# Kernel optimization log

Measured on AMD Instinct MI355X. Metric: run time of the kernel, lower is better.

## Reference

```python
import jax, jax.numpy as jnp
import numpy as np

B, N, C = 4, 2048, 320
H, D = 5, 64            # heads, dim_head
INNER = H * D           # 320


def setup_inputs() -> dict:
    key = jax.random.key(0)
    ks = jax.random.split(key, 7)
    x = jax.random.normal(ks[0], (B, N, C), dtype=jnp.float32)
    edge = jax.random.uniform(ks[1], (B, N, 1), dtype=jnp.float32)
    s = 1.0 / np.sqrt(C)
    Wq = jax.random.normal(ks[2], (C, INNER), dtype=jnp.float32) * s
    Wk = jax.random.normal(ks[3], (C, INNER), dtype=jnp.float32) * s
    Wv = jax.random.normal(ks[4], (C, INNER), dtype=jnp.float32) * s
    Wo = jax.random.normal(ks[5], (INNER, C), dtype=jnp.float32) * (1.0 / np.sqrt(INNER))
    bo = jnp.zeros((C,), dtype=jnp.float32)
    return {"x": x, "edge": edge, "Wq": Wq, "Wk": Wk, "Wv": Wv, "Wo": Wo, "bo": bo}


def _split_heads(t):
    # 'b n (h d) -> (b h) n d'  (batch-major, head-minor)
    b, n, _ = t.shape
    return t.reshape(b, n, H, D).transpose(0, 2, 1, 3).reshape(b * H, n, D)


def reference(x, edge, Wq, Wk, Wv, Wo, bo):
    scale = D ** -0.5
    q = _split_heads(x @ Wq).astype(jnp.float32)   # (B*H, N, D)
    k = _split_heads(x @ Wk).astype(jnp.float32)
    v = _split_heads(x @ Wv)

    sim = jnp.einsum('bid,bjd->bij', q, k) * scale  # (B*H, N, N)

    # torch: edge.repeat(h, 1, 1) -> batch-minor tiling; index i uses edge[i % B]
    edge_rep = jnp.tile(edge, (H, 1, 1))            # (H*B, N, 1)
    edge_matrix = edge_rep * edge_rep.transpose(0, 2, 1)  # outer product (H*B, N, N)

    sim = jax.nn.softmax(sim * edge_matrix, axis=-1)
    out = jnp.einsum('bij,bjd->bid', sim, v)        # (B*H, N, D)

    # '(b h) n d -> b n (h d)'
    out = out.reshape(B, H, N, D).transpose(0, 2, 1, 3).reshape(B, N, INNER)
    return out @ Wo + bo
```

## Files before the change

### kernel.cpp

```cpp
#include <hip/hip_runtime.h>
#include <hip/hip_bf16.h>
#include <math.h>


typedef short bf16x8 __attribute__((ext_vector_type(8)));
typedef float f32x4 __attribute__((ext_vector_type(4)));

static __device__ __forceinline__ ushort f2bf(float f) {
  union { float f; unsigned u; } v; v.f = f;
  unsigned r = (v.u + 0x7fffu + ((v.u >> 16) & 1u)) >> 16;
  return (ushort)r;
}
static __device__ __forceinline__ float fexp2(float x) {
#if __has_builtin(__builtin_amdgcn_exp2f)
  return __builtin_amdgcn_exp2f(x);
#else
  return exp2f(x);
#endif
}
static __device__ __forceinline__ f32x4 mfma32(bf16x8 a, bf16x8 b, f32x4 c) {
  return __builtin_amdgcn_mfma_f32_16x16x32_bf16(a, b, c, 0, 0, 0);
}

__global__ __launch_bounds__(256) void prep_kernel(
    const float* __restrict__ x,
    const float* __restrict__ Wq, const float* __restrict__ Wk,
    const float* __restrict__ Wv, const float* __restrict__ Wo,
    ushort* __restrict__ xb, ushort* __restrict__ wt)
{
  const int w = blockIdx.x;
  if (w < 2560) {
    const int t = threadIdx.x;
    const int mt2 = w / 5;
    const int kc = (w % 5) * 2 + (t >> 7);
    const int f = (t & 127) * 4;
    const int qq = f >> 7, mm = (f >> 3) & 15, e0 = f & 7;
    float4 v = *reinterpret_cast<const float4*>(
        x + (size_t)(mt2 * 16 + mm) * 320 + kc * 32 + qq * 8 + e0);
    ushort4 o = { f2bf(v.x), f2bf(v.y), f2bf(v.z), f2bf(v.w) };
    *reinterpret_cast<ushort4*>(xb + (size_t)(mt2 * 10 + kc) * 512 + f) = o;
  } else {
    const int w2 = w - 2560;
    const int nt2 = w2 % 20, kc = (w2 / 20) % 10, z = w2 / 200;
    const float* W = z == 0 ? Wq : z == 1 ? Wk : z == 2 ? Wv : Wo;
    const int f = threadIdx.x * 2;
    const int qq = f >> 7, nn = (f >> 3) & 15, e0 = f & 7;
    const int k = kc * 32 + qq * 8 + e0, n = nt2 * 16 + nn;
    float v0 = W[(size_t)k * 320 + n];
    float v1 = W[(size_t)(k + 1) * 320 + n];
    ushort2 o = { f2bf(v0), f2bf(v1) };
    *reinterpret_cast<ushort2*>(
        wt + (size_t)z * 102400 + (size_t)(nt2 * 10 + kc) * 512 + f) = o;
  }
}

__global__ __launch_bounds__(256, 3) void qkv_gemm(
    const ushort* __restrict__ xb, const float* __restrict__ edge,
    const ushort* __restrict__ wt,
    ushort* __restrict__ qp, ushort* __restrict__ kS, ushort* __restrict__ vS)
{
  const int w = blockIdx.x;
  const int s = (w & 7) * 60 + (w >> 3);
  const int mg = s / 15, zh = s % 15;
  const int z = zh / 5, h = zh % 5;
  const int wave = threadIdx.x >> 6, lane = threadIdx.x & 63;
  const int m16 = lane & 15, quad = lane >> 4;
  const int m0 = mg * 256 + wave * 64;
  const ushort* atile = xb + (size_t)(m0 >> 4) * 5120 + lane * 8;
  const ushort* btile = wt + (size_t)z * 102400 + (size_t)(h * 4) * 5120 + lane * 8;

  f32x4 acc[4][4];
#pragma unroll
  for (int i = 0; i < 4; ++i)
#pragma unroll
    for (int ns = 0; ns < 4; ++ns) acc[i][ns] = (f32x4){0.f, 0.f, 0.f, 0.f};

#pragma unroll
  for (int kc = 0; kc < 10; ++kc) {
    bf16x8 af[4], bf[4];
#pragma unroll
    for (int i = 0; i < 4; ++i)
      af[i] = *reinterpret_cast<const bf16x8*>(atile + (i * 10 + kc) * 512);
#pragma unroll
    for (int ns = 0; ns < 4; ++ns)
      bf[ns] = *reinterpret_cast<const bf16x8*>(btile + (ns * 10 + kc) * 512);
    if (z == 2) {
#pragma unroll
      for (int i = 0; i < 4; ++i)
#pragma unroll
        for (int ns = 0; ns < 4; ++ns)
          acc[i][ns] = mfma32(af[i], bf[ns], acc[i][ns]);
    } else {
#pragma unroll
      for (int i = 0; i < 4; ++i)
#pragma unroll
        for (int ns = 0; ns < 4; ++ns)
          acc[i][ns] = mfma32(bf[ns], af[i], acc[i][ns]);
    }
  }

  const float QSCALE = 0.18033688011112042f;
  const int b = m0 >> 11;
  const int bh = b * 5 + h;
  const float* eb = edge + (size_t)((b + h) & 3) * 2048;
  const int nwb = m0 & 2047;

  if (z == 0) {
#pragma unroll
    for (int i = 0; i < 4; ++i) {
      const int n = nwb + i * 16 + m16;
      const float e = eb[n] * QSCALE;
      ushort* dst = qp + ((size_t)bh * 2048 + n) * 64 + quad * 4;
#pragma unroll
      for (int ns = 0; ns < 4; ++ns) {
        ushort4 o = { f2bf(acc[i][ns][0] * e), f2bf(acc[i][ns][1] * e),
                      f2bf(acc[i][ns][2] * e), f2bf(acc[i][ns][3] * e) };
        *reinterpret_cast<ushort4*>(dst + ns * 16) = o;
      }
    }
  } else if (z == 1) {
#pragma unroll
    for (int i = 0; i < 4; ++i) {
      const int j = nwb + i * 16 + m16;
      const float e = eb[j];
      const size_t base = (size_t)bh * 131072 +
                          (size_t)((m0 >> 4) + i & 127) * 1024;
#pragma unroll
      for (int ns = 0; ns < 4; ++ns) {
        size_t a0 = base + (ns >> 1) * 512 +
                    ((((ns * 2 + (quad >> 1)) & 3) * 16 + m16)) * 8 +
                    (quad & 1) * 4;
        ushort4 o = { f2bf(acc[i][ns][0] * e), f2bf(acc[i][ns][1] * e),
                      f2bf(acc[i][ns][2] * e), f2bf(acc[i][ns][3] * e) };
        *reinterpret_cast<ushort4*>(kS + a0) = o;
      }
    }
  } else {
    const int jb = nwb >> 6;
#pragma unroll
    for (int i = 0; i < 4; ++i) {
      const int kb = i >> 1, e4 = (i & 1) * 4;
#pragma unroll
      for (int ns = 0; ns < 4; ++ns) {
        ushort4 o = { f2bf(acc[i][ns][0]), f2bf(acc[i][ns][1]),
                      f2bf(acc[i][ns][2]), f2bf(acc[i][ns][3]) };
        size_t addr = (size_t)bh * 131072 + (size_t)ns * 32768 +
                      (size_t)jb * 1024 + kb * 512 +
                      (quad * 16 + m16) * 8 + e4;
        *reinterpret_cast<ushort4*>(vS + addr) = o;
      }
    }
  }
}

__global__ __launch_bounds__(256, 3) void attn_kernel(
    const ushort* __restrict__ qp, const ushort* __restrict__ kS,
    const ushort* __restrict__ vS, ushort* __restrict__ ao)
{
  __shared__ f32x4 lo[3][16][64];
  __shared__ float lrs[4][4][16];
  const int w = blockIdx.x;
  const int s = (w & 7) * 80 + (w >> 3);
  const int bh = s >> 5, qt = s & 31;
  const int b = bh / 5, h = bh % 5;
  const int wave = threadIdx.x >> 6, lane = threadIdx.x & 63;
  const int m16 = lane & 15, quad = lane >> 4;
  const int q0 = qt * 64;

  bf16x8 qf[4][2];
#pragma unroll
  for (int qs = 0; qs < 4; ++qs) {
    const ushort* qrow = qp + ((size_t)bh * 2048 + q0 + qs * 16 + m16) * 64;
    qf[qs][0] = *reinterpret_cast<const bf16x8*>(qrow + quad * 8);
    qf[qs][1] = *reinterpret_cast<const bf16x8*>(qrow + 32 + quad * 8);
  }
  const ushort* kb_p = kS + (size_t)bh * 131072 + (size_t)wave * 32768 + lane * 8;
  const ushort* vb_p = vS + (size_t)bh * 131072 + (size_t)wave * 8192 + lane * 8;

  f32x4 oacc[4][4];
  float rs[4];
#pragma unroll
  for (int qs = 0; qs < 4; ++qs) {
    rs[qs] = 0.f;
#pragma unroll
    for (int dt = 0; dt < 4; ++dt) oacc[qs][dt] = (f32x4){0.f, 0.f, 0.f, 0.f};
  }

#pragma unroll 2
  for (int u = 0; u < 16; ++u) {
    bf16x8 kf[2][2], vf[4];
#pragma unroll
    for (int ss = 0; ss < 2; ++ss)
#pragma unroll
      for (int hf = 0; hf < 2; ++hf)
        kf[ss][hf] = *reinterpret_cast<const bf16x8*>(
            kb_p + (size_t)u * 2048 + ss * 1024 + hf * 512);
#pragma unroll
    for (int dt = 0; dt < 4; ++dt)
      vf[dt] = *reinterpret_cast<const bf16x8*>(
          vb_p + (size_t)dt * 32768 + (size_t)u * 512);

#pragma unroll
    for (int qs = 0; qs < 4; ++qs) {
      f32x4 st0 = (f32x4){0.f, 0.f, 0.f, 0.f};
      f32x4 st1 = (f32x4){0.f, 0.f, 0.f, 0.f};
      st0 = mfma32(kf[0][0], qf[qs][0], st0);
      st0 = mfma32(kf[0][1], qf[qs][1], st0);
      st1 = mfma32(kf[1][0], qf[qs][0], st1);
      st1 = mfma32(kf[1][1], qf[qs][1], st1);
      unsigned b0 = __float_as_uint(fexp2(st0[0]));
      unsigned b1 = __float_as_uint(fexp2(st0[1]));
      unsigned b2 = __float_as_uint(fexp2(st0[2]));
      unsigned b3 = __float_as_uint(fexp2(st0[3]));
      unsigned b4 = __float_as_uint(fexp2(st1[0]));
      unsigned b5 = __float_as_uint(fexp2(st1[1]));
      unsigned b6 = __float_as_uint(fexp2(st1[2]));
      unsigned b7 = __float_as_uint(fexp2(st1[3]));
      float t0 = __uint_as_float(b0 & 0xffff0000u);
      float t1 = __uint_as_float(b1 & 0xffff0000u);
      float t2 = __uint_as_float(b2 & 0xffff0000u);
      float t3 = __uint_as_float(b3 & 0xffff0000u);
      float t4 = __uint_as_float(b4 & 0xffff0000u);
      float t5 = __uint_as_float(b5 & 0xffff0000u);
      float t6 = __uint_as_float(b6 & 0xffff0000u);
      float t7 = __uint_as_float(b7 & 0xffff0000u);
      rs[qs] += ((t0 + t1) + (t2 + t3)) + ((t4 + t5) + (t6 + t7));
      union { unsigned u[4]; bf16x8 v; } pk;
      pk.u[0] = __builtin_amdgcn_perm(b1, b0, 0x07060302u);
      pk.u[1] = __builtin_amdgcn_perm(b3, b2, 0x07060302u);
      pk.u[2] = __builtin_amdgcn_perm(b5, b4, 0x07060302u);
      pk.u[3] = __builtin_amdgcn_perm(b7, b6, 0x07060302u);
#pragma unroll
      for (int dt = 0; dt < 4; ++dt)
        oacc[qs][dt] = mfma32(vf[dt], pk.v, oacc[qs][dt]);
    }
  }

#pragma unroll
  for (int qs = 0; qs < 4; ++qs) {
    float r = rs[qs];
    r += __shfl_xor(r, 16, 64);
    r += __shfl_xor(r, 32, 64);
    rs[qs] = r;
  }

  if (wave > 0) {
#pragma unroll
    for (int qs = 0; qs < 4; ++qs)
#pragma unroll
      for (int dt = 0; dt < 4; ++dt)
        lo[wave - 1][qs * 4 + dt][lane] = oacc[qs][dt];
  }
  if (quad == 0) {
#pragma unroll
    for (int qs = 0; qs < 4; ++qs) lrs[wave][qs][m16] = rs[qs];
  }
  __syncthreads();
  if (wave == 0) {
#pragma unroll
    for (int qs = 0; qs < 4; ++qs) {
      float inv = 1.0f / (lrs[0][qs][m16] + lrs[1][qs][m16] +
                          lrs[2][qs][m16] + lrs[3][qs][m16]);
      const int mt2 = b * 128 + qt * 4 + qs;
#pragma unroll
      for (int dt = 0; dt < 4; ++dt) {
        f32x4 a = oacc[qs][dt];
        a += lo[0][qs * 4 + dt][lane];
        a += lo[1][qs * 4 + dt][lane];
        a += lo[2][qs * 4 + dt][lane];
        unsigned r0 = f2bf(a[0] * inv), r1 = f2bf(a[1] * inv);
        unsigned r2 = f2bf(a[2] * inv), r3 = f2bf(a[3] * inv);
        uint2 ww;
        ww.x = r0 | (r1 << 16);
        ww.y = r2 | (r3 << 16);
        size_t addr = (size_t)(mt2 * 10 + h * 2 + (dt >> 1)) * 512 +
                      ((((dt & 1) * 2 + (quad >> 1)) * 16 + m16)) * 8 +
                      (quad & 1) * 4;
        *reinterpret_cast<uint2*>(ao + addr) = ww;
      }
    }
  }
}

__global__ __launch_bounds__(256, 3) void oproj_gemm(
    const ushort* __restrict__ ao, const ushort* __restrict__ wt,
    const float* __restrict__ bo, float* __restrict__ out)
{
  const int w = blockIdx.x;
  const int s = (w & 7) * 40 + (w >> 3);
  const int mg = s / 5, ct = s % 5;
  const int wave = threadIdx.x >> 6, lane = threadIdx.x & 63;
  const int m16 = lane & 15, quad = lane >> 4;
  const int m0 = mg * 128 + wave * 32;
  const int n0 = ct * 64;
  const ushort* atile = ao + (size_t)(m0 >> 4) * 5120 + lane * 8;
  const ushort* btile = wt + (size_t)3 * 102400 + (size_t)(ct * 4) * 5120 + lane * 8;

  f32x4 acc[2][4];
#pragma unroll
  for (int i = 0; i < 2; ++i)
#pragma unroll
    for (int ns = 0; ns < 4; ++ns) acc[i][ns] = (f32x4){0.f, 0.f, 0.f, 0.f};

#pragma unroll
  for (int kc = 0; kc < 10; ++kc) {
    bf16x8 af[2], bf[4];
#pragma unroll
    for (int i = 0; i < 2; ++i)
      af[i] = *reinterpret_cast<const bf16x8*>(atile + (i * 10 + kc) * 512);
#pragma unroll
    for (int ns = 0; ns < 4; ++ns)
      bf[ns] = *reinterpret_cast<const bf16x8*>(btile + (ns * 10 + kc) * 512);
#pragma unroll
    for (int i = 0; i < 2; ++i)
#pragma unroll
      for (int ns = 0; ns < 4; ++ns)
        acc[i][ns] = mfma32(bf[ns], af[i], acc[i][ns]);
  }

  float4 bb[4];
#pragma unroll
  for (int ns = 0; ns < 4; ++ns)
    bb[ns] = *reinterpret_cast<const float4*>(bo + n0 + ns * 16 + quad * 4);
#pragma unroll
  for (int i = 0; i < 2; ++i) {
    const int mrow = m0 + i * 16 + m16;
#pragma unroll
    for (int ns = 0; ns < 4; ++ns) {
      float4 o;
      o.x = acc[i][ns][0] + bb[ns].x;
      o.y = acc[i][ns][1] + bb[ns].y;
      o.z = acc[i][ns][2] + bb[ns].z;
      o.w = acc[i][ns][3] + bb[ns].w;
      *reinterpret_cast<float4*>(
          out + (size_t)mrow * 320 + n0 + ns * 16 + quad * 4) = o;
    }
  }
}

extern "C" void kernel_launch(void* const* d_in, const int* in_sizes, int n_in,
                              void* d_out, int out_size, void* d_ws, size_t ws_size,
                              hipStream_t stream) {
  const float* x    = (const float*)d_in[0];
  const float* edge = (const float*)d_in[1];
  const float* Wq   = (const float*)d_in[2];
  const float* Wk   = (const float*)d_in[3];
  const float* Wv   = (const float*)d_in[4];
  const float* Wo   = (const float*)d_in[5];
  const float* bo   = (const float*)d_in[6];
  float* out = (float*)d_out;

  ushort* xb = (ushort*)d_ws;
  ushort* wt = xb + (size_t)8192 * 320;
  ushort* qp = wt + (size_t)4 * 320 * 320;
  ushort* kS = qp + (size_t)20 * 2048 * 64;
  ushort* vS = kS + (size_t)20 * 2048 * 64;
  ushort* ao = vS + (size_t)20 * 2048 * 64;

  prep_kernel<<<3360, 256, 0, stream>>>(x, Wq, Wk, Wv, Wo, xb, wt);
  qkv_gemm<<<480, 256, 0, stream>>>(xb, edge, wt, qp, kS, vS);
  attn_kernel<<<640, 256, 0, stream>>>(qp, kS, vS, ao);
  oproj_gemm<<<320, 256, 0, stream>>>(ao, wt, bo, out);
}
```

Measured before the change: 140.3 us.

## Restructure attention to per-wave query rows with LDS double-buffered K/V tiles

Before this change, each of the four waves processed all 64 query rows over a quarter of the keys, and the partial outputs and row sums were reduced across waves through LDS at the end. Now each wave owns 16 query rows and iterates over all keys. K/V tiles are cooperatively staged into a double-buffered shared-memory ring with direct global-to-LDS loads, so the block reads each K/V tile once and shares it. This removes the cross-wave reduction and cuts register pressure, allowing the launch bound to rise from 3 to 4 blocks. The cost is a __syncthreads per key tile, an LDS read per fragment, and four times as many outer iterations per wave.

```diff
diff --git a/kernel.cpp b/kernel.cpp
--- a/kernel.cpp
+++ b/kernel.cpp
@@ -21,6 +21,11 @@
 static __device__ __forceinline__ f32x4 mfma32(bf16x8 a, bf16x8 b, f32x4 c) {
   return __builtin_amdgcn_mfma_f32_16x16x32_bf16(a, b, c, 0, 0, 0);
 }
+
+#define GLD_LDS16(gsrc, ldst)                                                  \
+  __builtin_amdgcn_global_load_lds(                                            \
+      (const __attribute__((address_space(1))) unsigned int*)(gsrc),           \
+      (__attribute__((address_space(3))) unsigned int*)(ldst), 16, 0, 0)
 
 __global__ __launch_bounds__(256) void prep_kernel(
     const float* __restrict__ x,
@@ -153,12 +158,11 @@
   }
 }
 
-__global__ __launch_bounds__(256, 3) void attn_kernel(
+__global__ __launch_bounds__(256, 4) void attn_kernel(
     const ushort* __restrict__ qp, const ushort* __restrict__ kS,
     const ushort* __restrict__ vS, ushort* __restrict__ ao)
 {
-  __shared__ f32x4 lo[3][16][64];
-  __shared__ float lrs[4][4][16];
+  __shared__ ushort sm[16384];
   const int w = blockIdx.x;
   const int s = (w & 7) * 80 + (w >> 3);
   const int bh = s >> 5, qt = s & 31;
@@ -167,47 +171,61 @@
   const int m16 = lane & 15, quad = lane >> 4;
   const int q0 = qt * 64;
 
-  bf16x8 qf[4][2];
-#pragma unroll
-  for (int qs = 0; qs < 4; ++qs) {
-    const ushort* qrow = qp + ((size_t)bh * 2048 + q0 + qs * 16 + m16) * 64;
-    qf[qs][0] = *reinterpret_cast<const bf16x8*>(qrow + quad * 8);
-    qf[qs][1] = *reinterpret_cast<const bf16x8*>(qrow + 32 + quad * 8);
-  }
-  const ushort* kb_p = kS + (size_t)bh * 131072 + (size_t)wave * 32768 + lane * 8;
-  const ushort* vb_p = vS + (size_t)bh * 131072 + (size_t)wave * 8192 + lane * 8;
-
-  f32x4 oacc[4][4];
-  float rs[4];
-#pragma unroll
-  for (int qs = 0; qs < 4; ++qs) {
-    rs[qs] = 0.f;
-#pragma unroll
-    for (int dt = 0; dt < 4; ++dt) oacc[qs][dt] = (f32x4){0.f, 0.f, 0.f, 0.f};
-  }
-
-#pragma unroll 2
-  for (int u = 0; u < 16; ++u) {
-    bf16x8 kf[2][2], vf[4];
-#pragma unroll
-    for (int ss = 0; ss < 2; ++ss)
-#pragma unroll
-      for (int hf = 0; hf < 2; ++hf)
-        kf[ss][hf] = *reinterpret_cast<const bf16x8*>(
-            kb_p + (size_t)u * 2048 + ss * 1024 + hf * 512);
-#pragma unroll
-    for (int dt = 0; dt < 4; ++dt)
-      vf[dt] = *reinterpret_cast<const bf16x8*>(
-          vb_p + (size_t)dt * 32768 + (size_t)u * 512);
-
-#pragma unroll
-    for (int qs = 0; qs < 4; ++qs) {
+  bf16x8 qf[2];
+  {
+    const ushort* qrow = qp + ((size_t)bh * 2048 + q0 + wave * 16 + m16) * 64;
+    qf[0] = *reinterpret_cast<const bf16x8*>(qrow + quad * 8);
+    qf[1] = *reinterpret_cast<const bf16x8*>(qrow + 32 + quad * 8);
+  }
+
+  const ushort* kbase = kS + (size_t)bh * 131072;
+  const ushort* vbase = vS + (size_t)bh * 131072;
+
+  f32x4 oacc[4];
+  float rs = 0.f;
+#pragma unroll
+  for (int dt = 0; dt < 4; ++dt) oacc[dt] = (f32x4){0.f, 0.f, 0.f, 0.f};
+
+  auto stage = [&](int jt, int buf) {
+    const ushort* ks = kbase + (size_t)jt * 4096 + wave * 1024 + lane * 8;
+    const ushort* vs = vbase + (size_t)wave * 32768 + (size_t)jt * 1024 + lane * 8;
+    ushort* dk = &sm[buf * 8192 + wave * 1024];
+    ushort* dv = &sm[buf * 8192 + 4096 + wave * 1024];
+#pragma unroll
+    for (int is = 0; is < 2; ++is) {
+      GLD_LDS16(ks + is * 512, dk + is * 512);
+      GLD_LDS16(vs + is * 512, dv + is * 512);
+    }
+  };
+
+  stage(0, 0);
+  __syncthreads();
+
+  int cur = 0;
+  for (int jt = 0; jt < 32; ++jt) {
+    if (jt < 31) stage(jt + 1, cur ^ 1);
+    const ushort* kb0 = &sm[cur * 8192];
+    const ushort* vb0 = &sm[cur * 8192 + 4096];
+#pragma unroll
+    for (int uu = 0; uu < 2; ++uu) {
+      bf16x8 kf[2][2], vf[4];
+#pragma unroll
+      for (int ss = 0; ss < 2; ++ss)
+#pragma unroll
+        for (int hf = 0; hf < 2; ++hf)
+          kf[ss][hf] = *reinterpret_cast<const bf16x8*>(
+              kb0 + uu * 2048 + ss * 1024 + hf * 512 + lane * 8);
+#pragma unroll
+      for (int dt = 0; dt < 4; ++dt)
+        vf[dt] = *reinterpret_cast<const bf16x8*>(
+            vb0 + dt * 1024 + uu * 512 + lane * 8);
+
       f32x4 st0 = (f32x4){0.f, 0.f, 0.f, 0.f};
       f32x4 st1 = (f32x4){0.f, 0.f, 0.f, 0.f};
-      st0 = mfma32(kf[0][0], qf[qs][0], st0);
-      st0 = mfma32(kf[0][1], qf[qs][1], st0);
-      st1 = mfma32(kf[1][0], qf[qs][0], st1);
-      st1 = mfma32(kf[1][1], qf[qs][1], st1);
+      st0 = mfma32(kf[0][0], qf[0], st0);
+      st0 = mfma32(kf[0][1], qf[1], st0);
+      st1 = mfma32(kf[1][0], qf[0], st1);
+      st1 = mfma32(kf[1][1], qf[1], st1);
       unsigned b0 = __float_as_uint(fexp2(st0[0]));
       unsigned b1 = __float_as_uint(fexp2(st0[1]));
       unsigned b2 = __float_as_uint(fexp2(st0[2]));
@@ -224,7 +242,7 @@
       float t5 = __uint_as_float(b5 & 0xffff0000u);
       float t6 = __uint_as_float(b6 & 0xffff0000u);
       float t7 = __uint_as_float(b7 & 0xffff0000u);
-      rs[qs] += ((t0 + t1) + (t2 + t3)) + ((t4 + t5) + (t6 + t7));
+      rs += ((t0 + t1) + (t2 + t3)) + ((t4 + t5) + (t6 + t7));
       union { unsigned u[4]; bf16x8 v; } pk;
       pk.u[0] = __builtin_amdgcn_perm(b1, b0, 0x07060302u);
       pk.u[1] = __builtin_amdgcn_perm(b3, b2, 0x07060302u);
@@ -232,53 +250,29 @@
       pk.u[3] = __builtin_amdgcn_perm(b7, b6, 0x07060302u);
 #pragma unroll
       for (int dt = 0; dt < 4; ++dt)
-        oacc[qs][dt] = mfma32(vf[dt], pk.v, oacc[qs][dt]);
-    }
-  }
-
-#pragma unroll
-  for (int qs = 0; qs < 4; ++qs) {
-    float r = rs[qs];
-    r += __shfl_xor(r, 16, 64);
-    r += __shfl_xor(r, 32, 64);
-    rs[qs] = r;
-  }
-
-  if (wave > 0) {
-#pragma unroll
-    for (int qs = 0; qs < 4; ++qs)
-#pragma unroll
-      for (int dt = 0; dt < 4; ++dt)
-        lo[wave - 1][qs * 4 + dt][lane] = oacc[qs][dt];
-  }
-  if (quad == 0) {
-#pragma unroll
-    for (int qs = 0; qs < 4; ++qs) lrs[wave][qs][m16] = rs[qs];
-  }
-  __syncthreads();
-  if (wave == 0) {
-#pragma unroll
-    for (int qs = 0; qs < 4; ++qs) {
-      float inv = 1.0f / (lrs[0][qs][m16] + lrs[1][qs][m16] +
-                          lrs[2][qs][m16] + lrs[3][qs][m16]);
-      const int mt2 = b * 128 + qt * 4 + qs;
-#pragma unroll
-      for (int dt = 0; dt < 4; ++dt) {
-        f32x4 a = oacc[qs][dt];
-        a += lo[0][qs * 4 + dt][lane];
-        a += lo[1][qs * 4 + dt][lane];
-        a += lo[2][qs * 4 + dt][lane];
-        unsigned r0 = f2bf(a[0] * inv), r1 = f2bf(a[1] * inv);
-        unsigned r2 = f2bf(a[2] * inv), r3 = f2bf(a[3] * inv);
-        uint2 ww;
-        ww.x = r0 | (r1 << 16);
-        ww.y = r2 | (r3 << 16);
-        size_t addr = (size_t)(mt2 * 10 + h * 2 + (dt >> 1)) * 512 +
-                      ((((dt & 1) * 2 + (quad >> 1)) * 16 + m16)) * 8 +
-                      (quad & 1) * 4;
-        *reinterpret_cast<uint2*>(ao + addr) = ww;
-      }
-    }
+        oacc[dt] = mfma32(vf[dt], pk.v, oacc[dt]);
+    }
+    __syncthreads();
+    cur ^= 1;
+  }
+
+  rs += __shfl_xor(rs, 16, 64);
+  rs += __shfl_xor(rs, 32, 64);
+  const float inv = 1.0f / rs;
+
+  const int mt2 = b * 128 + qt * 4 + wave;
+#pragma unroll
+  for (int dt = 0; dt < 4; ++dt) {
+    f32x4 a = oacc[dt];
+    unsigned r0 = f2bf(a[0] * inv), r1 = f2bf(a[1] * inv);
+    unsigned r2 = f2bf(a[2] * inv), r3 = f2bf(a[3] * inv);
+    uint2 ww;
+    ww.x = r0 | (r1 << 16);
+    ww.y = r2 | (r3 << 16);
+    size_t addr = (size_t)(mt2 * 10 + h * 2 + (dt >> 1)) * 512 +
+                  ((((dt & 1) * 2 + (quad >> 1)) * 16 + m16)) * 8 +
+                  (quad & 1) * 4;
+    *reinterpret_cast<uint2*>(ao + addr) = ww;
   }
 }
 
```

New measurement: 128.1 us. -8.7%, faster.
